# Performance work log

Measured on AMD Instinct MI355X. Metric: run time of the kernel, lower is better.

Reference implementation:

```python
import jax, jax.numpy as jnp
import numpy as np

ATT_K = 180   # attention_k
NPOOL = 15    # WeldonPooling(15): mean of top-15 + mean of bottom-15 spatial scores


def setup_inputs() -> dict:
    key = jax.random.key(0)
    k1, k2, k3, k4 = jax.random.split(key, 4)
    imgs, emb, h, w = 16, 2400, 14, 14
    caps_cnt = 64
    return {
        "g": jax.random.normal(k1, (imgs, emb, h, w), dtype=jnp.float32),
        "caps": jax.random.normal(k2, (caps_cnt, emb), dtype=jnp.float32),
        "fc_w": jax.random.normal(k3, (emb, emb), dtype=jnp.float32) * 0.02,
        "fc_b": jax.random.normal(k4, (emb,), dtype=jnp.float32) * 0.02,
    }


def reference(g, caps, fc_w, fc_b):
    imgs, emb, h, w = g.shape
    caps_cnt = caps.shape[0]

    # ---- WeldonPooling(15): per (img, channel) sort spatial scores ----
    flat = g.reshape(imgs, emb, h * w)
    s = jnp.sort(flat, axis=2)  # ascending
    hpool = s[:, :, -NPOOL:].mean(axis=2) + s[:, :, :NPOOL].mean(axis=2)  # [imgs, emb]
    x = hpool @ fc_w.T + fc_b  # fc (dropout is identity at eval / p=0)

    # ---- get_heat_map: top-k caption dims, gather fc-projected features ----
    order = jnp.argsort(-caps, axis=1)[:, :ATT_K]                 # [C, k] indices
    vals = jnp.take_along_axis(caps, order, axis=1)               # [C, k] top-k values (desc)
    gf = jnp.einsum('oe,iehw->oihw', fc_w, g)                     # fc.weight @ g -> [emb, imgs, h, w]
    gsel = gf[order]                                              # gather -> [C, k, imgs, h, w]
    heat = jnp.sum(jnp.abs(gsel * vals[:, :, None, None, None]), axis=1)  # [C, imgs, h, w]
    heat = jnp.transpose(heat, (1, 0, 2, 3))                      # [imgs, C, h, w]
    heat = heat / jnp.sum(heat, axis=(2, 3), keepdims=True)       # normalize per (img, cap)

    # ---- attention_embedding: weighted spatial sum, then fc ----
    xa = jnp.einsum('ichw,iehw->ice', heat, g)                    # [imgs, C, emb]
    xa = xa @ fc_w.T + fc_b

    return x, xa, g
```

## Files before the change

### kernel.cpp

```cpp
#include <hip/hip_runtime.h>
#include <math.h>

#define IMGS 16
#define EMB 2400
#define HW 196
#define CAPS 64
#define ATTK 180
#define NPOOL 15
#define NCOLS (IMGS * HW)
#define KPAD 224

typedef __attribute__((ext_vector_type(8))) short short8;
typedef __attribute__((ext_vector_type(4))) float f32x4;
typedef const __attribute__((address_space(1))) unsigned int* gas1_t;
typedef __attribute__((address_space(3))) unsigned int* las3_t;
typedef unsigned long long ull;

__device__ inline unsigned short f2bf(float f) {
    unsigned int u = __builtin_bit_cast(unsigned int, f);
    u += 0x7fffu + ((u >> 16) & 1u);
    return (unsigned short)(u >> 16);
}
__device__ inline float bf2f(unsigned int lo16) {
    return __builtin_bit_cast(float, lo16 << 16);
}
__device__ inline unsigned f2sort(float f) {
    unsigned u = __builtin_bit_cast(unsigned, f);
    int msk = ((int)u) >> 31;
    return u ^ (unsigned)(msk | 0x80000000);
}

__global__ __launch_bounds__(256) void weldon_kernel(const float* __restrict__ g,
                                                     float* __restrict__ hpool) {
    int wid = (blockIdx.x * 256 + threadIdx.x) >> 6;
    int tlane = threadIdx.x & 63;
    int hl = tlane & 31;
    bool neg = tlane >= 32;
    const float* row = g + (size_t)wid * HW;
    float s[7];
#pragma unroll
    for (int q = 0; q < 7; q++) {
        int e = hl + 32 * q;
        if (e < HW) {
            unsigned u = __builtin_bit_cast(unsigned, row[e]);
            if (neg) u ^= 0x80000000u;
            u = (u & 0xFFFFFF00u) | (unsigned)(q * 32 + hl);
            s[q] = __builtin_bit_cast(float, u);
        } else {
            s[q] = -INFINITY;
        }
    }
#define CS(a, b)                                   \
    {                                              \
        float hi = fmaxf(s[a], s[b]);              \
        float lo = fminf(s[a], s[b]);              \
        s[a] = hi; s[b] = lo;                      \
    }
    CS(1, 2) CS(3, 4) CS(5, 6)
    CS(0, 2) CS(3, 5) CS(4, 6)
    CS(0, 1) CS(4, 5) CS(2, 6)
    CS(0, 4) CS(1, 5)
    CS(0, 3) CS(2, 5)
    CS(1, 3) CS(2, 4)
    CS(2, 3)
#undef CS
    float acc = 0.f;
#pragma unroll
    for (int it = 0; it < NPOOL; ++it) {
        int x = __builtin_bit_cast(int, s[0]);
#define ST(c)                                                                  \
    {                                                                          \
        int y = __builtin_amdgcn_update_dpp(x, x, c, 0xf, 0xf, false);         \
        float a = fmaxf(__builtin_bit_cast(float, x), __builtin_bit_cast(float, y)); \
        x = __builtin_bit_cast(int, a);                                        \
    }
        ST(0x111) ST(0x112) ST(0x114) ST(0x118) ST(0x142)
#undef ST
        int m31 = __builtin_amdgcn_readlane(x, 31);
        int m63 = __builtin_amdgcn_readlane(x, 63);
        float msel = __builtin_bit_cast(float, neg ? m63 : m31);
        acc += msel;
        bool won = (__builtin_bit_cast(unsigned, s[0]) ==
                    __builtin_bit_cast(unsigned, msel));
        s[0] = won ? s[1] : s[0];
        s[1] = won ? s[2] : s[1];
        s[2] = won ? s[3] : s[2];
        s[3] = won ? s[4] : s[3];
        s[4] = won ? s[5] : s[4];
        s[5] = won ? s[6] : s[5];
        s[6] = won ? -INFINITY : s[6];
    }
    int ai = __builtin_bit_cast(int, acc);
    float a0 = __builtin_bit_cast(float, __builtin_amdgcn_readlane(ai, 0));
    float a32 = __builtin_bit_cast(float, __builtin_amdgcn_readlane(ai, 32));
    if (tlane == 0) hpool[wid] = (a0 - a32) / 15.0f;
}

__global__ void xw_kernel(const float* __restrict__ hpool, const float* __restrict__ fc_w,
                          const float* __restrict__ fc_b, float* __restrict__ x_out,
                          unsigned short* __restrict__ wbf) {
    int o = blockIdx.x;
    int lane = threadIdx.x;
    float acc[IMGS];
#pragma unroll
    for (int i = 0; i < IMGS; i++) acc[i] = 0.f;
    const float* wrow = fc_w + (size_t)o * EMB;
    unsigned short* wdst = wbf + (size_t)o * EMB;
    for (int e = lane * 4; e < EMB; e += 256) {
        float4 wv = *(const float4*)&wrow[e];
        ushort4 r;
        r.x = f2bf(wv.x); r.y = f2bf(wv.y); r.z = f2bf(wv.z); r.w = f2bf(wv.w);
        *(ushort4*)&wdst[e] = r;
#pragma unroll
        for (int i = 0; i < IMGS; i++) {
            const float* hp = hpool + i * EMB + e;
            acc[i] += hp[0] * wv.x + hp[1] * wv.y + hp[2] * wv.z + hp[3] * wv.w;
        }
    }
#pragma unroll
    for (int i = 0; i < IMGS; i++) {
#pragma unroll
        for (int sdx = 32; sdx > 0; sdx >>= 1) acc[i] += __shfl_xor(acc[i], sdx, 64);
    }
    if (lane == 0) {
        float bo = fc_b[o];
#pragma unroll
        for (int i = 0; i < IMGS; i++) x_out[i * EMB + o] = acc[i] + bo;
    }
}

__global__ void x_kernel(const float* __restrict__ hpool, const float* __restrict__ fc_w,
                         const float* __restrict__ fc_b, float* __restrict__ x_out) {
    int o = blockIdx.x;
    int lane = threadIdx.x;
    float acc[IMGS];
#pragma unroll
    for (int i = 0; i < IMGS; i++) acc[i] = 0.f;
    const float* wrow = fc_w + (size_t)o * EMB;
    for (int e = lane; e < EMB; e += 64) {
        float wv = wrow[e];
#pragma unroll
        for (int i = 0; i < IMGS; i++) acc[i] += hpool[i * EMB + e] * wv;
    }
#pragma unroll
    for (int i = 0; i < IMGS; i++) {
#pragma unroll
        for (int sdx = 32; sdx > 0; sdx >>= 1) acc[i] += __shfl_xor(acc[i], sdx, 64);
    }
    if (lane == 0) {
        float bo = fc_b[o];
#pragma unroll
        for (int i = 0; i < IMGS; i++) x_out[i * EMB + o] = acc[i] + bo;
    }
}

__global__ __launch_bounds__(256) void topk_kernel(const float* __restrict__ caps,
                                                   int* __restrict__ idxs,
                                                   float* __restrict__ vals) {
    __shared__ float rowf[EMB];
    __shared__ unsigned hist[4][256];
    __shared__ unsigned scanbuf[256];
    __shared__ unsigned cnts[256];
    __shared__ ull sprefix;
    __shared__ int srank;
    int c = blockIdx.x;
    int tid = threadIdx.x;
    const float4* src = (const float4*)(caps + (size_t)c * EMB);
    for (int j = tid; j < EMB / 4; j += 256) {
        float4 v = src[j];
        *(float4*)&rowf[j * 4] = v;
    }
    if (tid == 0) { sprefix = 0ull; srank = ATTK; }

#pragma unroll 1
    for (int pass = 0; pass < 6; ++pass) {
        __syncthreads();
        ull pref = sprefix;
        int rk = srank;
        int shift = 40 - pass * 8;
        ull pmaskhi = (pass == 0) ? 0ull : ~((1ull << (shift + 8)) - 1ull);
        hist[0][tid] = 0; hist[1][tid] = 0; hist[2][tid] = 0; hist[3][tid] = 0;
        __syncthreads();
        unsigned* myhist = hist[tid >> 6];
#pragma unroll 1
        for (int s = 0; s < 10; s++) {
            int e = tid + s * 256;
            if (e < EMB) {
                ull key = ((ull)f2sort(rowf[e]) << 16) | ((unsigned)(2399 - e) << 4);
                if ((key & pmaskhi) == pref)
                    atomicAdd(&myhist[(unsigned)(key >> shift) & 255u], 1u);
            }
        }
        __syncthreads();
        unsigned h = hist[0][tid] + hist[1][tid] + hist[2][tid] + hist[3][tid];
        scanbuf[255 - tid] = h;
        __syncthreads();
#pragma unroll
        for (int d = 1; d < 256; d <<= 1) {
            unsigned add = (tid >= d) ? scanbuf[tid - d] : 0u;
            __syncthreads();
            scanbuf[tid] += add;
            __syncthreads();
        }
        unsigned incl = scanbuf[255 - tid];
        unsigned excl = incl - h;
        if (h > 0u && excl < (unsigned)rk && incl >= (unsigned)rk) {
            srank = rk - (int)excl;
            sprefix = pref | ((ull)tid << shift);
        }
    }
    __syncthreads();
    ull T = sprefix;
    unsigned selmask = 0, cnt = 0;
#pragma unroll 1
    for (int s = 0; s < 10; s++) {
        int e = tid + s * 256;
        if (e < EMB) {
            ull key = ((ull)f2sort(rowf[e]) << 16) | ((unsigned)(2399 - e) << 4);
            if (key >= T) { selmask |= 1u << s; cnt++; }
        }
    }
    cnts[tid] = cnt;
    __syncthreads();
#pragma unroll
    for (int d = 1; d < 256; d <<= 1) {
        unsigned add = (tid >= d) ? cnts[tid - d] : 0u;
        __syncthreads();
        cnts[tid] += add;
        __syncthreads();
    }
    unsigned slot = cnts[tid] - cnt;
#pragma unroll 1
    for (int s = 0; s < 10; s++) {
        if (selmask & (1u << s)) {
            int e = tid + s * 256;
            idxs[c * ATTK + slot] = e;
            vals[c * ATTK + slot] = fabsf(rowf[e]);
            slot++;
        }
    }
}

__global__ void transpose_g_kernel(const float* __restrict__ g, unsigned short* __restrict__ gT) {
    __shared__ float t[96][50];
    int i = blockIdx.z;
    int e0 = blockIdx.y * 96;
    int h0 = blockIdx.x * 49;
    int tid = threadIdx.x;
    for (int f = tid; f < 96 * 49; f += 256) {
        int e = f / 49, hh = f % 49;
        t[e][hh] = g[(size_t)i * EMB * HW + (size_t)(e0 + e) * HW + h0 + hh];
    }
    __syncthreads();
    for (int f = tid; f < 49 * 96; f += 256) {
        int hh = f / 96, e = f % 96;
        gT[(size_t)(i * HW + h0 + hh) * EMB + e0 + e] = f2bf(t[e][hh]);
    }
}

template <int MF, int NF, int OUT_MODE>
__global__ __launch_bounds__(256) void gemm_gll(const unsigned short* __restrict__ A,
                                                const unsigned short* __restrict__ B,
                                                void* __restrict__ outp,
                                                const float* __restrict__ bias,
                                                const float* __restrict__ invS,
                                                int M, int N, int K, int ldb, int kper,
                                                long az, long bz) {
    constexpr int BM = MF * 32, BN = NF * 32;
    constexpr int ROWS = BM + BN;
    constexpr int RPAD = (ROWS + 63) & ~63;
    constexpr int NCALL = RPAD / 16;
    constexpr int LPW = NCALL / 4;
    __shared__ unsigned short lds[3][RPAD][32];
    int gx = gridDim.x, gy = gridDim.y;
    int nwg = gx * gy;
    int flat = blockIdx.y * gx + blockIdx.x;
    int qq = nwg >> 3, rr8 = nwg & 7;
    int xcd = flat & 7, idx = flat >> 3;
    int base = (xcd < rr8) ? xcd * (qq + 1) : rr8 * (qq + 1) + (xcd - rr8) * qq;
    int nf = base + idx;
    int m0 = (nf % gy) * BM;
    int n0 = (nf / gy) * BN;
    int z = blockIdx.z;
    const unsigned short* Ab = A + (size_t)z * az;
    const unsigned short* Bb = B + (size_t)z * bz;
    int kb = (az == 0 && bz == 0) ? z * kper : 0;
    int nt = kper / 32;
    int tid = threadIdx.x, w = tid >> 6, lane = tid & 63;
    int wm = (w >> 1) * (MF * 16), wn = (w & 1) * (NF * 16);
    int ln = lane & 15;
    int ks = (((lane >> 4) ^ ((lane >> 1) & 3))) * 8;
    int srow = lane >> 2;
    int skc = (((lane & 3) ^ ((lane >> 3) & 3))) * 8;

    auto STAGE = [&](int buf, int t) {
        int k0 = kb + t * 32;
#pragma unroll
        for (int j = 0; j < LPW; j++) {
            int jj = w + j * 4;
            int r = jj * 16 + srow;
            const unsigned short* src;
            if (r < BM) src = Ab + (size_t)(m0 + r) * K + k0 + skc;
            else if (r < ROWS) src = Bb + (size_t)(n0 + r - BM) * ldb + k0 + skc;
            else src = Ab + (size_t)m0 * K + k0 + skc;
            __builtin_amdgcn_global_load_lds((gas1_t)(const void*)src,
                                             (las3_t)(void*)&lds[buf][jj * 16][0], 16, 0, 0);
        }
    };

    STAGE(0, 0);
    if (nt > 1) STAGE(1, 1);
    f32x4 acc[MF][NF] = {};
    for (int t = 0; t < nt; ++t) {
        if (t + 1 < nt) {
            if constexpr (LPW == 4) asm volatile("s_waitcnt vmcnt(4) lgkmcnt(0)" ::: "memory");
            else if constexpr (LPW == 5) asm volatile("s_waitcnt vmcnt(5) lgkmcnt(0)" ::: "memory");
            else if constexpr (LPW == 6) asm volatile("s_waitcnt vmcnt(6) lgkmcnt(0)" ::: "memory");
            else asm volatile("s_waitcnt vmcnt(0) lgkmcnt(0)" ::: "memory");
        } else {
            asm volatile("s_waitcnt vmcnt(0) lgkmcnt(0)" ::: "memory");
        }
        __builtin_amdgcn_s_barrier();
        __builtin_amdgcn_sched_barrier(0);
        if (t + 2 < nt) STAGE((t + 2) % 3, t + 2);
        const unsigned short(*buf)[32] = lds[t % 3];
        short8 af[MF], bfv[NF];
#pragma unroll
        for (int mf = 0; mf < MF; mf++)
            af[mf] = *(const short8*)&buf[wm + mf * 16 + ln][ks];
#pragma unroll
        for (int nfi = 0; nfi < NF; nfi++)
            bfv[nfi] = *(const short8*)&buf[BM + wn + nfi * 16 + ln][ks];
        __builtin_amdgcn_s_setprio(1);
#pragma unroll
        for (int mf = 0; mf < MF; mf++)
#pragma unroll
            for (int nfi = 0; nfi < NF; nfi++)
                acc[mf][nfi] = __builtin_amdgcn_mfma_f32_16x16x32_bf16(af[mf], bfv[nfi],
                                                                       acc[mf][nfi], 0, 0, 0);
        __builtin_amdgcn_s_setprio(0);
    }
#pragma unroll
    for (int mf = 0; mf < MF; mf++) {
#pragma unroll
        for (int nfi = 0; nfi < NF; nfi++) {
#pragma unroll
            for (int rr = 0; rr < 4; rr++) {
                int row = m0 + wm + mf * 16 + (lane >> 4) * 4 + rr;
                int col = n0 + wn + nfi * 16 + ln;
                float v = acc[mf][nfi][rr];
                if (OUT_MODE == 6) {
                    ((unsigned short*)outp)[(size_t)row * N + col] = f2bf(v);
                } else if (OUT_MODE == 4) {
                    ((float*)outp)[((size_t)z * CAPS + row) * N + col] =
                        v * invS[z * CAPS + row] + bias[col];
                }
            }
        }
    }
}

__device__ inline uint4 load8(const unsigned short* p) { return *(const uint4*)p; }
__device__ inline uint4 load8(const float* p) {
    float4 a = *(const float4*)p;
    float4 b = *(const float4*)(p + 4);
    uint4 r;
    r.x = (unsigned)f2bf(a.x) | ((unsigned)f2bf(a.y) << 16);
    r.y = (unsigned)f2bf(a.z) | ((unsigned)f2bf(a.w) << 16);
    r.z = (unsigned)f2bf(b.x) | ((unsigned)f2bf(b.y) << 16);
    r.w = (unsigned)f2bf(b.z) | ((unsigned)f2bf(b.w) << 16);
    return r;
}

template <int MF, int NF, typename TA, typename TB>
__global__ __launch_bounds__(256) void mfma_gemm_nt(const TA* __restrict__ A,
                                                    const TB* __restrict__ B,
                                                    void* __restrict__ outp,
                                                    int M, int N, int K) {
    constexpr int BM = MF * 32, BN = NF * 32;
    constexpr int nA = BM * 4, nTot = (BM + BN) * 4;
    constexpr int NCH = (nTot + 255) / 256;
    __shared__ unsigned short As[BM][40];
    __shared__ unsigned short Bs[BN][40];
    int m0 = blockIdx.y * BM, n0 = blockIdx.x * BN;
    int tid = threadIdx.x;
    int w = tid >> 6, lane = tid & 63;
    int wm = (w >> 1) * (MF * 16), wn = (w & 1) * (NF * 16);
    int ln = lane & 15, ks = (lane >> 4) * 8;
    uint4 r[NCH];
#pragma unroll
    for (int j = 0; j < NCH; j++) {
        int c = tid + 256 * j;
        if (c < nTot) {
            if (c < nA) {
                int row = c >> 2, kc = c & 3;
                r[j] = load8(A + (size_t)(m0 + row) * K + kc * 8);
            } else {
                int cc = c - nA, row = cc >> 2, kc = cc & 3;
                r[j] = load8(B + (size_t)(n0 + row) * K + kc * 8);
            }
        }
    }
    f32x4 acc[MF][NF] = {};
    for (int k0 = 0; k0 < K; k0 += 32) {
#pragma unroll
        for (int j = 0; j < NCH; j++) {
            int c = tid + 256 * j;
            if (c < nTot) {
                if (c < nA) {
                    int row = c >> 2, kc = c & 3;
                    *(uint4*)&As[row][kc * 8] = r[j];
                } else {
                    int cc = c - nA, row = cc >> 2, kc = cc & 3;
                    *(uint4*)&Bs[row][kc * 8] = r[j];
                }
            }
        }
        __syncthreads();
        if (k0 + 32 < K) {
#pragma unroll
            for (int j = 0; j < NCH; j++) {
                int c = tid + 256 * j;
                if (c < nTot) {
                    if (c < nA) {
                        int row = c >> 2, kc = c & 3;
                        r[j] = load8(A + (size_t)(m0 + row) * K + (k0 + 32) + kc * 8);
                    } else {
                        int cc = c - nA, row = cc >> 2, kc = cc & 3;
                        r[j] = load8(B + (size_t)(n0 + row) * K + (k0 + 32) + kc * 8);
                    }
                }
            }
        }
        short8 af[MF], bfv[NF];
#pragma unroll
        for (int mf = 0; mf < MF; mf++)
            af[mf] = *(const short8*)&As[wm + mf * 16 + ln][ks];
#pragma unroll
        for (int nfi = 0; nfi < NF; nfi++)
            bfv[nfi] = *(const short8*)&Bs[wn + nfi * 16 + ln][ks];
#pragma unroll
        for (int mf = 0; mf < MF; mf++)
#pragma unroll
            for (int nfi = 0; nfi < NF; nfi++)
                acc[mf][nfi] = __builtin_amdgcn_mfma_f32_16x16x32_bf16(af[mf], bfv[nfi],
                                                                       acc[mf][nfi], 0, 0, 0);
        __syncthreads();
    }
#pragma unroll
    for (int mf = 0; mf < MF; mf++) {
#pragma unroll
        for (int nfi = 0; nfi < NF; nfi++) {
#pragma unroll
            for (int rr = 0; rr < 4; rr++) {
                int row = m0 + wm + mf * 16 + (lane >> 4) * 4 + rr;
                int col = n0 + wn + nfi * 16 + ln;
                ((unsigned short*)outp)[(size_t)row * N + col] = f2bf(acc[mf][nfi][rr]);
            }
        }
    }
}

__global__ __launch_bounds__(256) void heat_kernel(const int* __restrict__ idxs,
                                                   const float* __restrict__ vals,
                                                   const unsigned short* __restrict__ A,
                                                   unsigned short* __restrict__ Hnbf) {
    __shared__ int sidx[ATTK];
    __shared__ float sval[ATTK];
    int c = blockIdx.y;
    int tid = threadIdx.x;
    if (tid < ATTK) {
        sidx[tid] = idxs[c * ATTK + tid];
        sval[tid] = vals[c * ATTK + tid];
    }
    __syncthreads();
    int n = blockIdx.x * 256 + tid;
    if (n >= NCOLS) return;
    float a0 = 0.f, a1 = 0.f, a2 = 0.f, a3 = 0.f;
#pragma unroll 1
    for (int j = 0; j < ATTK; j += 4) {
        a0 += sval[j + 0] * bf2f(A[(size_t)sidx[j + 0] * NCOLS + n] & 0x7FFFu);
        a1 += sval[j + 1] * bf2f(A[(size_t)sidx[j + 1] * NCOLS + n] & 0x7FFFu);
        a2 += sval[j + 2] * bf2f(A[(size_t)sidx[j + 2] * NCOLS + n] & 0x7FFFu);
        a3 += sval[j + 3] * bf2f(A[(size_t)sidx[j + 3] * NCOLS + n] & 0x7FFFu);
    }
    int i = n / HW, hw = n % HW;
    Hnbf[((size_t)i * CAPS + c) * KPAD + hw] = f2bf((a0 + a1) + (a2 + a3));
}

__global__ void rowsum_kernel(const unsigned short* __restrict__ Hnbf,
                              float* __restrict__ invS) {
    int b = blockIdx.x;
    int lane = threadIdx.x;
    const unsigned short* p = Hnbf + (size_t)b * KPAD;
    float s = bf2f(p[lane]) + bf2f(p[lane + 64]) + bf2f(p[lane + 128]);
    if (lane < 32) s += bf2f(p[lane + 192]);
#pragma unroll
    for (int d = 32; d > 0; d >>= 1) s += __shfl_xor(s, d, 64);
    if (lane == 0) invS[b] = 1.0f / s;
}

extern "C" void kernel_launch(void* const* d_in, const int* in_sizes, int n_in,
                              void* d_out, int out_size, void* d_ws, size_t ws_size,
                              hipStream_t stream) {
    const float* g = (const float*)d_in[0];
    const float* caps = (const float*)d_in[1];
    const float* fc_w = (const float*)d_in[2];
    const float* fc_b = (const float*)d_in[3];

    float* out = (float*)d_out;
    float* x_out = out;
    float* xa_out = out + 38400;
    float* g_out = out + 38400 + 2457600;
    unsigned short* Asig = (unsigned short*)g_out;
    unsigned short* gT = Asig + (size_t)EMB * NCOLS;

    float* ws = (float*)d_ws;
    float* hpool = ws;
    int* idxs = (int*)(ws + 38400);
    float* vals = ws + 49920;
    float* invS = ws + 61440;
    unsigned short* Hnbf = (unsigned short*)(ws + 62464);
    unsigned short* wbf = (unsigned short*)(ws + 1490944);
    bool use_wbf = ws_size >= (size_t)17483776;

    weldon_kernel<<<(IMGS * EMB) / 4, 256, 0, stream>>>(g, hpool);
    topk_kernel<<<CAPS, 256, 0, stream>>>(caps, idxs, vals);
    transpose_g_kernel<<<dim3(4, 25, IMGS), 256, 0, stream>>>(g, gT);

    if (use_wbf) {
        xw_kernel<<<EMB, 64, 0, stream>>>(hpool, fc_w, fc_b, x_out, wbf);
        gemm_gll<5, 7, 6><<<dim3(NCOLS / 224, EMB / 160, 1), 256, 0, stream>>>(
            wbf, gT, Asig, nullptr, nullptr, EMB, NCOLS, EMB, EMB, EMB, 0, 0);
    } else {
        x_kernel<<<EMB, 64, 0, stream>>>(hpool, fc_w, fc_b, x_out);
        mfma_gemm_nt<5, 2, float, unsigned short>
            <<<dim3(NCOLS / 64, EMB / 160), 256, 0, stream>>>(fc_w, gT, Asig,
                                                              EMB, NCOLS, EMB);
    }
    hipMemsetAsync(Hnbf, 0, sizeof(unsigned short) * (size_t)IMGS * CAPS * KPAD, stream);
    heat_kernel<<<dim3((NCOLS + 255) / 256, CAPS), 256, 0, stream>>>(idxs, vals, Asig, Hnbf);
    rowsum_kernel<<<IMGS * CAPS, 64, 0, stream>>>(Hnbf, invS);
    gemm_gll<2, 5, 4><<<dim3(EMB / 160, 1, IMGS), 256, 0, stream>>>(
        Hnbf, Asig, xa_out, fc_b, invS, CAPS, EMB, KPAD, NCOLS, KPAD,
        (long)CAPS * KPAD, HW);
    hipMemcpyAsync(g_out, g, sizeof(float) * (size_t)IMGS * EMB * HW,
                   hipMemcpyDeviceToDevice, stream);
}
```

Measured before the change: 173.1 us.

## Fuse weldon pooling with g transpose; fold rowsum and memset into heat kernel

New measurement: 165.8 us. 1.04x faster.

```diff
diff --git a/kernel.cpp b/kernel.cpp
--- a/kernel.cpp
+++ b/kernel.cpp
@@ -30,70 +30,86 @@
     return u ^ (unsigned)(msk | 0x80000000);
 }
 
-__global__ __launch_bounds__(256) void weldon_kernel(const float* __restrict__ g,
-                                                     float* __restrict__ hpool) {
-    int wid = (blockIdx.x * 256 + threadIdx.x) >> 6;
-    int tlane = threadIdx.x & 63;
-    int hl = tlane & 31;
-    bool neg = tlane >= 32;
-    const float* row = g + (size_t)wid * HW;
-    float s[7];
-#pragma unroll
-    for (int q = 0; q < 7; q++) {
-        int e = hl + 32 * q;
-        if (e < HW) {
-            unsigned u = __builtin_bit_cast(unsigned, row[e]);
-            if (neg) u ^= 0x80000000u;
-            u = (u & 0xFFFFFF00u) | (unsigned)(q * 32 + hl);
-            s[q] = __builtin_bit_cast(float, u);
-        } else {
-            s[q] = -INFINITY;
-        }
-    }
+__global__ __launch_bounds__(256) void transpool_kernel(const float* __restrict__ g,
+                                                        float* __restrict__ hpool,
+                                                        unsigned short* __restrict__ gT) {
+    __shared__ float t[32][197];
+    int e0 = blockIdx.x * 32;
+    int i = blockIdx.y;
+    int tid = threadIdx.x;
+    const float* base = g + ((size_t)i * EMB + e0) * HW;
+    for (int f = tid; f < 32 * HW; f += 256) {
+        int e = f / HW, hw = f % HW;
+        t[e][hw] = base[(size_t)e * HW + hw];
+    }
+    __syncthreads();
+    for (int f = tid; f < HW * 32; f += 256) {
+        int hw = f / 32, e = f % 32;
+        gT[((size_t)i * HW + hw) * EMB + e0 + e] = f2bf(t[e][hw]);
+    }
+    int w = tid >> 6, tl = tid & 63, hl = tl & 31;
+    bool negh = tl >= 32;
+#pragma unroll 1
+    for (int rr = 0; rr < 8; ++rr) {
+        int e = w * 8 + rr;
+        float s[7];
+#pragma unroll
+        for (int q = 0; q < 7; q++) {
+            int hw = hl + 32 * q;
+            if (hw < HW) {
+                unsigned u = __builtin_bit_cast(unsigned, t[e][hw]);
+                if (negh) u ^= 0x80000000u;
+                u = (u & 0xFFFFFF00u) | (unsigned)(q * 32 + hl);
+                s[q] = __builtin_bit_cast(float, u);
+            } else {
+                s[q] = -INFINITY;
+            }
+        }
 #define CS(a, b)                                   \
     {                                              \
         float hi = fmaxf(s[a], s[b]);              \
         float lo = fminf(s[a], s[b]);              \
         s[a] = hi; s[b] = lo;                      \
     }
-    CS(1, 2) CS(3, 4) CS(5, 6)
-    CS(0, 2) CS(3, 5) CS(4, 6)
-    CS(0, 1) CS(4, 5) CS(2, 6)
-    CS(0, 4) CS(1, 5)
-    CS(0, 3) CS(2, 5)
-    CS(1, 3) CS(2, 4)
-    CS(2, 3)
+        CS(1, 2) CS(3, 4) CS(5, 6)
+        CS(0, 2) CS(3, 5) CS(4, 6)
+        CS(0, 1) CS(4, 5) CS(2, 6)
+        CS(0, 4) CS(1, 5)
+        CS(0, 3) CS(2, 5)
+        CS(1, 3) CS(2, 4)
+        CS(2, 3)
 #undef CS
-    float acc = 0.f;
-#pragma unroll
-    for (int it = 0; it < NPOOL; ++it) {
-        int x = __builtin_bit_cast(int, s[0]);
+        float acc = 0.f;
+#pragma unroll
+        for (int it = 0; it < NPOOL; ++it) {
+            int x = __builtin_bit_cast(int, s[0]);
 #define ST(c)                                                                  \
     {                                                                          \
         int y = __builtin_amdgcn_update_dpp(x, x, c, 0xf, 0xf, false);         \
         float a = fmaxf(__builtin_bit_cast(float, x), __builtin_bit_cast(float, y)); \
         x = __builtin_bit_cast(int, a);                                        \
     }
-        ST(0x111) ST(0x112) ST(0x114) ST(0x118) ST(0x142)
+            ST(0x111) ST(0x112) ST(0x114) ST(0x118) ST(0x142)
 #undef ST
-        int m31 = __builtin_amdgcn_readlane(x, 31);
-        int m63 = __builtin_amdgcn_readlane(x, 63);
-        float msel = __builtin_bit_cast(float, neg ? m63 : m31);
-        acc += msel;
-        bool won = (__builtin_bit_cast(unsigned, s[0]) ==
-                    __builtin_bit_cast(unsigned, msel));
-        s[0] = won ? s[1] : s[0];
-        s[1] = won ? s[2] : s[1];
-        s[2] = won ? s[3] : s[2];
-        s[3] = won ? s[4] : s[3];
-        s[4] = won ? s[5] : s[4];
-        s[5] = won ? s[6] : s[5];
-        s[6] = won ? -INFINITY : s[6];
-    }
-    int ai = __builtin_bit_cast(int, acc);
-    float a0 = __builtin_bit_cast(float, __builtin_amdgcn_readlane(ai, 0));
-    float a32 = __builtin_bit_cast(float, __builtin_amdgcn_readlane(ai, 32));
-    if (tlane == 0) hpool[wid] = (a0 - a32) / 15.0f;
+            int m31 = __builtin_amdgcn_readlane(x, 31);
+            int m63 = __builtin_amdgcn_readlane(x, 63);
+            float msel = __builtin_bit_cast(float, negh ? m63 : m31);
+            acc += msel;
+            bool won = (__builtin_bit_cast(unsigned, s[0]) ==
+                        __builtin_bit_cast(unsigned, msel));
+            s[0] = won ? s[1] : s[0];
+            s[1] = won ? s[2] : s[1];
+            s[2] = won ? s[3] : s[2];
+            s[3] = won ? s[4] : s[3];
+            s[4] = won ? s[5] : s[4];
+            s[5] = won ? s[6] : s[5];
+            s[6] = won ? -INFINITY : s[6];
+        }
+        int ai = __builtin_bit_cast(int, acc);
+        float a0 = __builtin_bit_cast(float, __builtin_amdgcn_readlane(ai, 0));
+        float a32 = __builtin_bit_cast(float, __builtin_amdgcn_readlane(ai, 32));
+        if (tl == 0) hpool[(size_t)i * EMB + e0 + e] = (a0 - a32) / 15.0f;
+    }
 }
 
 __global__ void xw_kernel(const float* __restrict__ hpool, const float* __restrict__ fc_w,
@@ -160,11 +176,12 @@
     __shared__ float rowf[EMB];
     __shared__ unsigned hist[4][256];
     __shared__ unsigned scanbuf[256];
-    __shared__ unsigned cnts[256];
+    __shared__ unsigned wtot[4];
     __shared__ ull sprefix;
     __shared__ int srank;
     int c = blockIdx.x;
     int tid = threadIdx.x;
+    int w = tid >> 6, lane = tid & 63;
     const float4* src = (const float4*)(caps + (size_t)c * EMB);
     for (int j = tid; j < EMB / 4; j += 256) {
         float4 v = src[j];
@@ -181,7 +198,7 @@
         ull pmaskhi = (pass == 0) ? 0ull : ~((1ull << (shift + 8)) - 1ull);
         hist[0][tid] = 0; hist[1][tid] = 0; hist[2][tid] = 0; hist[3][tid] = 0;
         __syncthreads();
-        unsigned* myhist = hist[tid >> 6];
+        unsigned* myhist = hist[w];
 #pragma unroll 1
         for (int s = 0; s < 10; s++) {
             int e = tid + s * 256;
@@ -195,13 +212,18 @@
         unsigned h = hist[0][tid] + hist[1][tid] + hist[2][tid] + hist[3][tid];
         scanbuf[255 - tid] = h;
         __syncthreads();
-#pragma unroll
-        for (int d = 1; d < 256; d <<= 1) {
-            unsigned add = (tid >= d) ? scanbuf[tid - d] : 0u;
-            __syncthreads();
-            scanbuf[tid] += add;
-            __syncthreads();
-        }
+        unsigned x = scanbuf[tid];
+#pragma unroll
+        for (int d = 1; d < 64; d <<= 1) {
+            unsigned u = __shfl_up(x, d, 64);
+            if (lane >= d) x += u;
+        }
+        if (lane == 63) wtot[w] = x;
+        __syncthreads();
+        unsigned off = 0;
+        for (int ww = 0; ww < w; ww++) off += wtot[ww];
+        scanbuf[tid] = x + off;
+        __syncthreads();
         unsigned incl = scanbuf[255 - tid];
         unsigned excl = incl - h;
         if (h > 0u && excl < (unsigned)rk && incl >= (unsigned)rk) {
@@ -220,16 +242,17 @@
             if (key >= T) { selmask |= 1u << s; cnt++; }
         }
     }
-    cnts[tid] = cnt;
+    unsigned x = cnt;
+#pragma unroll
+    for (int d = 1; d < 64; d <<= 1) {
+        unsigned u = __shfl_up(x, d, 64);
+        if (lane >= d) x += u;
+    }
+    if (lane == 63) wtot[w] = x;
     __syncthreads();
-#pragma unroll
-    for (int d = 1; d < 256; d <<= 1) {
-        unsigned add = (tid >= d) ? cnts[tid - d] : 0u;
-        __syncthreads();
-        cnts[tid] += add;
-        __syncthreads();
-    }
-    unsigned slot = cnts[tid] - cnt;
+    unsigned off = 0;
+    for (int ww = 0; ww < w; ww++) off += wtot[ww];
+    unsigned slot = x + off - cnt;
 #pragma unroll 1
     for (int s = 0; s < 10; s++) {
         if (selmask & (1u << s)) {
@@ -238,23 +261,6 @@
             vals[c * ATTK + slot] = fabsf(rowf[e]);
             slot++;
         }
-    }
-}
-
-__global__ void transpose_g_kernel(const float* __restrict__ g, unsigned short* __restrict__ gT) {
-    __shared__ float t[96][50];
-    int i = blockIdx.z;
-    int e0 = blockIdx.y * 96;
-    int h0 = blockIdx.x * 49;
-    int tid = threadIdx.x;
-    for (int f = tid; f < 96 * 49; f += 256) {
-        int e = f / 49, hh = f % 49;
-        t[e][hh] = g[(size_t)i * EMB * HW + (size_t)(e0 + e) * HW + h0 + hh];
-    }
-    __syncthreads();
-    for (int f = tid; f < 49 * 96; f += 256) {
-        int hh = f / 96, e = f % 96;
-        gT[(size_t)(i * HW + h0 + hh) * EMB + e0 + e] = f2bf(t[e][hh]);
     }
 }
 
@@ -464,40 +470,42 @@
 __global__ __launch_bounds__(256) void heat_kernel(const int* __restrict__ idxs,
                                                    const float* __restrict__ vals,
                                                    const unsigned short* __restrict__ A,
-                                                   unsigned short* __restrict__ Hnbf) {
+                                                   unsigned short* __restrict__ Hnbf,
+                                                   float* __restrict__ invS) {
     __shared__ int sidx[ATTK];
     __shared__ float sval[ATTK];
-    int c = blockIdx.y;
+    __shared__ float wsum[4];
+    int i = blockIdx.x, c = blockIdx.y;
     int tid = threadIdx.x;
+    int w = tid >> 6, lane = tid & 63;
     if (tid < ATTK) {
         sidx[tid] = idxs[c * ATTK + tid];
         sval[tid] = vals[c * ATTK + tid];
     }
     __syncthreads();
-    int n = blockIdx.x * 256 + tid;
-    if (n >= NCOLS) return;
-    float a0 = 0.f, a1 = 0.f, a2 = 0.f, a3 = 0.f;
+    int hw = tid;
+    float v = 0.f;
+    if (hw < HW) {
+        int n = i * HW + hw;
+        float a0 = 0.f, a1 = 0.f, a2 = 0.f, a3 = 0.f;
 #pragma unroll 1
-    for (int j = 0; j < ATTK; j += 4) {
-        a0 += sval[j + 0] * bf2f(A[(size_t)sidx[j + 0] * NCOLS + n] & 0x7FFFu);
-        a1 += sval[j + 1] * bf2f(A[(size_t)sidx[j + 1] * NCOLS + n] & 0x7FFFu);
-        a2 += sval[j + 2] * bf2f(A[(size_t)sidx[j + 2] * NCOLS + n] & 0x7FFFu);
-        a3 += sval[j + 3] * bf2f(A[(size_t)sidx[j + 3] * NCOLS + n] & 0x7FFFu);
-    }
-    int i = n / HW, hw = n % HW;
-    Hnbf[((size_t)i * CAPS + c) * KPAD + hw] = f2bf((a0 + a1) + (a2 + a3));
-}
-
-__global__ void rowsum_kernel(const unsigned short* __restrict__ Hnbf,
-                              float* __restrict__ invS) {
-    int b = blockIdx.x;
-    int lane = threadIdx.x;
-    const unsigned short* p = Hnbf + (size_t)b * KPAD;
-    float s = bf2f(p[lane]) + bf2f(p[lane + 64]) + bf2f(p[lane + 128]);
-    if (lane < 32) s += bf2f(p[lane + 192]);
+        for (int j = 0; j < ATTK; j += 4) {
+            a0 += sval[j + 0] * bf2f(A[(size_t)sidx[j + 0] * NCOLS + n] & 0x7FFFu);
+            a1 += sval[j + 1] * bf2f(A[(size_t)sidx[j + 1] * NCOLS + n] & 0x7FFFu);
+            a2 += sval[j + 2] * bf2f(A[(size_t)sidx[j + 2] * NCOLS + n] & 0x7FFFu);
+            a3 += sval[j + 3] * bf2f(A[(size_t)sidx[j + 3] * NCOLS + n] & 0x7FFFu);
+        }
+        v = (a0 + a1) + (a2 + a3);
+    }
+    if (hw < KPAD)
+        Hnbf[((size_t)i * CAPS + c) * KPAD + hw] = (hw < HW) ? f2bf(v) : (unsigned short)0;
+    float s = v;
 #pragma unroll
     for (int d = 32; d > 0; d >>= 1) s += __shfl_xor(s, d, 64);
-    if (lane == 0) invS[b] = 1.0f / s;
+    if (lane == 0) wsum[w] = s;
+    __syncthreads();
+    if (tid == 0)
+        invS[i * CAPS + c] = 1.0f / (wsum[0] + wsum[1] + wsum[2] + wsum[3]);
 }
 
 extern "C" void kernel_launch(void* const* d_in, const int* in_sizes, int n_in,
@@ -524,9 +532,8 @@
     unsigned short* wbf = (unsigned short*)(ws + 1490944);
     bool use_wbf = ws_size >= (size_t)17483776;
 
-    weldon_kernel<<<(IMGS * EMB) / 4, 256, 0, stream>>>(g, hpool);
+    transpool_kernel<<<dim3(EMB / 32, IMGS), 256, 0, stream>>>(g, hpool, gT);
     topk_kernel<<<CAPS, 256, 0, stream>>>(caps, idxs, vals);
-    transpose_g_kernel<<<dim3(4, 25, IMGS), 256, 0, stream>>>(g, gT);
 
     if (use_wbf) {
         xw_kernel<<<EMB, 64, 0, stream>>>(hpool, fc_w, fc_b, x_out, wbf);
@@ -538,9 +545,7 @@
             <<<dim3(NCOLS / 64, EMB / 160), 256, 0, stream>>>(fc_w, gT, Asig,
                                                               EMB, NCOLS, EMB);
     }
-    hipMemsetAsync(Hnbf, 0, sizeof(unsigned short) * (size_t)IMGS * CAPS * KPAD, stream);
-    heat_kernel<<<dim3((NCOLS + 255) / 256, CAPS), 256, 0, stream>>>(idxs, vals, Asig, Hnbf);
-    rowsum_kernel<<<IMGS * CAPS, 64, 0, stream>>>(Hnbf, invS);
+    heat_kernel<<<dim3(IMGS, CAPS), 256, 0, stream>>>(idxs, vals, Asig, Hnbf, invS);
     gemm_gll<2, 5, 4><<<dim3(EMB / 160, 1, IMGS), 256, 0, stream>>>(
         Hnbf, Asig, xa_out, fc_b, invS, CAPS, EMB, KPAD, NCOLS, KPAD,
         (long)CAPS * KPAD, HW);
```
